# Performance work log

Hardware: AMD Instinct MI355X
Metric: run time of the kernel (lower is better)

The kernel has to match this reference:

```python
import jax, jax.numpy as jnp
import numpy as np

NUM_HEADS = 16
THETA = 10000.0


def setup_inputs() -> dict:
    key = jax.random.key(0)
    k1, k2, k3, k4 = jax.random.split(key, 4)
    B, T, D = 2, 2048, 1024
    x = jax.random.normal(k1, (B, T, D), dtype=jnp.float32)
    token_positions = jnp.sort(
        jax.random.randint(k2, (B, T), 0, 2048), axis=-1
    ).astype(jnp.int32)
    sigma_qkv = float(np.sqrt(2.0 / (D + 3 * D)))
    sigma_out = float(np.sqrt(2.0 / (D + D)))
    W_qkv = jax.random.normal(k3, (3 * D, D), dtype=jnp.float32) * sigma_qkv
    W_out = jax.random.normal(k4, (D, D), dtype=jnp.float32) * sigma_out
    return {"x": x, "token_positions": token_positions, "W_qkv": W_qkv, "W_out": W_out}


def _apply_rope(t, cos, sin):
    # t: [B, H, T, d_k]; cos/sin: [B, T, d_k//2]
    B, H, T, dk = t.shape
    t2 = t.reshape(B, H, T, dk // 2, 2)
    te, to = t2[..., 0], t2[..., 1]
    c = cos[:, None]  # [B, 1, T, dk//2]
    s = sin[:, None]
    ye = te * c - to * s
    yo = to * c + te * s
    return jnp.stack([ye, yo], axis=-1).reshape(B, H, T, dk)


def reference(x, token_positions, W_qkv, W_out):
    B, T, D = x.shape
    H = NUM_HEADS
    dk = D // H

    # fused QKV projection: [B, T, 3D] -> split (three, h, d) on last dim
    qkv = jnp.einsum("btd,od->bto", x, W_qkv).reshape(B, T, 3, H, dk)
    qkv = jnp.transpose(qkv, (2, 0, 3, 1, 4))  # [3, B, H, T, dk]
    q, k, v = qkv[0], qkv[1], qkv[2]

    # RoPE angles from token positions
    n = jnp.arange(dk // 2, dtype=jnp.float32)
    inv_freq = THETA ** (-2.0 * n / dk)  # [dk//2]
    angles = token_positions.astype(jnp.float32)[..., None] * inv_freq  # [B, T, dk//2]
    cos, sin = jnp.cos(angles), jnp.sin(angles)
    q = _apply_rope(q, cos, sin)
    k = _apply_rope(k, cos, sin)

    # causal scaled dot-product attention
    scores = jnp.einsum("bhid,bhjd->bhij", q, k) / jnp.sqrt(jnp.float32(dk))
    causal = jnp.tril(jnp.ones((T, T), dtype=bool))
    scores = jnp.where(causal, scores, -jnp.inf)
    probs = jax.nn.softmax(scores, axis=-1)
    attn = jnp.einsum("bhij,bhjd->bhid", probs, v)  # [B, H, T, dk]

    concat = jnp.transpose(attn, (0, 2, 1, 3)).reshape(B, T, D)
    return jnp.einsum("btd,od->bto", concat, W_out)
```

## Files before the change

### kernel.cpp

```cpp
#include <hip/hip_runtime.h>
#include <hip/hip_bf16.h>
#include <cmath>

#define T_SEQ 2048
#define D_MODEL 1024
#define NHEAD 16
#define DK 64

typedef short bf16x8 __attribute__((ext_vector_type(8)));
typedef float f32x4 __attribute__((ext_vector_type(4)));
typedef float f32x16 __attribute__((ext_vector_type(16)));
typedef unsigned uint2v __attribute__((ext_vector_type(2)));

union U8 { unsigned u[4]; bf16x8 v; };

__device__ __forceinline__ short f2b(float f) {
    unsigned u = __builtin_bit_cast(unsigned, f);
    unsigned r = (u + 0x7FFFu + ((u >> 16) & 1u)) >> 16;
    return (short)r;
}

__device__ __forceinline__ void gll16(const void* g, void* l) {
    __builtin_amdgcn_global_load_lds(
        (__attribute__((address_space(1))) void*)g,
        (__attribute__((address_space(3))) void*)l, 16, 0, 0);
}

__device__ __forceinline__ bf16x8 lds_frag(const short* base, int row, int chunk) {
    return *reinterpret_cast<const bf16x8*>(
        (const char*)base + row * 128 + ((chunk * 16) ^ ((row & 7) << 4)));
}

__device__ __forceinline__ unsigned pkbf16(float a, float b) {
    unsigned r;
    asm("v_cvt_pk_bf16_f32 %0, %1, %2" : "=v"(r) : "v"(a), "v"(b));
    return r;
}
__device__ __forceinline__ void pl32swap(unsigned& a, unsigned& b) {
    uint2v r = __builtin_amdgcn_permlane32_swap(a, b, false, false);
    a = r.x; b = r.y;
}

__global__ __launch_bounds__(256) void cvt_all(const float* __restrict__ x,
                                               const float* __restrict__ wq,
                                               const float* __restrict__ wo,
                                               short* __restrict__ xb,
                                               short* __restrict__ wqb,
                                               short* __restrict__ wob) {
    int i = blockIdx.x * 256 + threadIdx.x;
    const float* src;
    short* dst;
    int srcoff, c;
    if (i < 524288) {
        c = i;
        int tile = c >> 9, cc = c & 511;
        int kblk = cc >> 7, row = cc & 127;
        int rb = tile >> 5, kb = tile & 31;
        srcoff = (rb * 128 + row) * D_MODEL + kb * 32 + kblk * 8;
        src = x; dst = xb;
    } else if (i < 917504) {
        c = i - 524288;
        int tile = c >> 9, cc = c & 511;
        int kblk = cc >> 7, row = cc & 127;
        int rb = tile >> 5, kb = tile & 31;
        srcoff = (rb * 128 + row) * D_MODEL + kb * 32 + kblk * 8;
        src = wq; dst = wqb;
    } else {
        c = i - 917504;
        int tile = c >> 8, cc = c & 255;
        int kblk = cc >> 6, row = cc & 63;
        int nb = tile >> 5, kb = tile & 31;
        srcoff = (nb * 64 + row) * D_MODEL + kb * 32 + kblk * 8;
        src = wo; dst = wob;
    }
    float4 a = *reinterpret_cast<const float4*>(src + srcoff);
    float4 b = *reinterpret_cast<const float4*>(src + srcoff + 4);
    bf16x8 v;
    v[0] = f2b(a.x); v[1] = f2b(a.y); v[2] = f2b(a.z); v[3] = f2b(a.w);
    v[4] = f2b(b.x); v[5] = f2b(b.y); v[6] = f2b(b.z); v[7] = f2b(b.w);
    reinterpret_cast<bf16x8*>(dst)[c] = v;
}

__global__ __launch_bounds__(256) void rope_table(const int* __restrict__ pos,
                                                  float* __restrict__ ct,
                                                  float* __restrict__ st) {
    int i = blockIdx.x * blockDim.x + threadIdx.x;
    int bt = i >> 5, n = i & 31;
    float p = (float)pos[bt];
    float invf = expf((float)n * (-2.0f / (float)DK) * 9.210340371976184f);
    float ang = p * invf;
    float s, c;
    sincosf(ang, &s, &c);
    ct[i] = c; st[i] = s;
}

__global__ __launch_bounds__(256, 3) void gemm_qkv(const short* __restrict__ xb,
                                                   const short* __restrict__ wb,
                                                   const float* __restrict__ ct,
                                                   const float* __restrict__ st,
                                                   short* __restrict__ Qo,
                                                   short* __restrict__ Ko,
                                                   short* __restrict__ Vt) {
    __shared__ short As[2][4096];
    __shared__ short Bs[2][4096];
    const int tid = threadIdx.x;
    const int w = tid >> 6, l = tid & 63, lg = l >> 4, li = l & 15;
    const int wr = w >> 1, wc = w & 1;
    const int bn = blockIdx.x * 128, bm = blockIdx.y * 128;

    const short* pA = xb + (size_t)blockIdx.y * 32 * 4096 + (w * 128 + l) * 8;
    const short* pB = wb + (size_t)blockIdx.x * 32 * 4096 + (w * 128 + l) * 8;

    f32x4 zero = {0.f, 0.f, 0.f, 0.f};
    f32x4 acc[4][4];
#pragma unroll
    for (int m = 0; m < 4; ++m)
#pragma unroll
        for (int n = 0; n < 4; ++n) acc[m][n] = zero;

    gll16(pA,       &As[0][w * 1024]);
    gll16(pA + 512, &As[0][w * 1024 + 512]);
    gll16(pB,       &Bs[0][w * 1024]);
    gll16(pB + 512, &Bs[0][w * 1024 + 512]);
    __syncthreads();

    for (int t = 0; t < 32; ++t) {
        if (t < 31) {
            const int nb = (t + 1) & 1;
            const size_t ko = (size_t)(t + 1) * 4096;
            gll16(pA + ko,       &As[nb][w * 1024]);
            gll16(pA + ko + 512, &As[nb][w * 1024 + 512]);
            gll16(pB + ko,       &Bs[nb][w * 1024]);
            gll16(pB + ko + 512, &Bs[nb][w * 1024 + 512]);
        }
        const int cb = t & 1;
        bf16x8 a[4], b[4];
#pragma unroll
        for (int m = 0; m < 4; ++m)
            a[m] = *reinterpret_cast<const bf16x8*>(&As[cb][lg * 1024 + (wr * 64 + m * 16 + li) * 8]);
#pragma unroll
        for (int n = 0; n < 4; ++n)
            b[n] = *reinterpret_cast<const bf16x8*>(&Bs[cb][lg * 1024 + (wc * 64 + n * 16 + li) * 8]);
#pragma unroll
        for (int m = 0; m < 4; ++m)
#pragma unroll
            for (int n = 0; n < 4; ++n)
                acc[m][n] = __builtin_amdgcn_mfma_f32_16x16x32_bf16(a[m], b[n], acc[m][n], 0, 0, 0);
        __syncthreads();
    }

    const int which = bn >> 10;
    const int h = ((bn >> 6) + wc) & 15;
#pragma unroll
    for (int n = 0; n < 4; ++n) {
        const int d = n * 16 + li;
#pragma unroll
        for (int m = 0; m < 4; ++m)
#pragma unroll
            for (int r = 0; r < 4; ++r) {
                const int mi = bm + wr * 64 + m * 16 + lg * 4 + r;
                const int b_ = mi >> 11, tt = mi & (T_SEQ - 1);
                float v = acc[m][n][r];
                if (which == 2) {
                    Vt[((size_t)((b_ * NHEAD + h) * DK + d)) * T_SEQ + tt] = f2b(v);
                } else {
                    float vp = __shfl_xor(v, 1);
                    int nn = n * 8 + (li >> 1);
                    float c = ct[(size_t)mi * 32 + nn];
                    float s = st[(size_t)mi * 32 + nn];
                    float o = (d & 1) ? (v * c + vp * s) : (v * c - vp * s);
                    if (which == 0) o *= 0.18033688011112042f;
                    short* dst = (which == 0) ? Qo : Ko;
                    dst[((size_t)((b_ * NHEAD + h) * T_SEQ + tt)) * DK + d] = f2b(o);
                }
            }
    }
}

__global__ __launch_bounds__(256, 3) void attn(const short* __restrict__ Q,
                                               const short* __restrict__ K,
                                               const short* __restrict__ Vt,
                                               short* __restrict__ Cc) {
    __shared__ short Kls[2][4096];
    __shared__ short Vls[2][4096];

    const int bid = blockIdx.x;
    const int ii = bid & 255, rr = bid >> 8;
    const int bh = ii & 31;
    const int qt = rr ? (15 - (ii >> 5)) : (ii >> 5);
    const int blkq0 = qt * 128;
    const int ntb = 2 * qt + 2;

    const int tid = threadIdx.x;
    const int w = tid >> 6, l = tid & 63;
    const int l31 = l & 31, hi = l >> 5, hi4 = hi * 4, hi8 = hi * 8;
    const int q0w = blkq0 + w * 32;

    const short* Qh = Q + (size_t)bh * T_SEQ * DK;
    const short* Kh = K + (size_t)bh * T_SEQ * DK;
    const short* Vh = Vt + (size_t)bh * DK * T_SEQ;

    bf16x8 qf[4];
#pragma unroll
    for (int ks = 0; ks < 4; ++ks)
        qf[ks] = *reinterpret_cast<const bf16x8*>(&Qh[(size_t)(q0w + l31) * DK + ks * 16 + hi8]);

    f32x16 o0 = {0.f,0.f,0.f,0.f,0.f,0.f,0.f,0.f,0.f,0.f,0.f,0.f,0.f,0.f,0.f,0.f};
    f32x16 o1 = o0;
    float m = -3.0e38f;
    float lsum = 0.f;

    const int c0 = (2 * w) * 64 + l;
    const int c1 = c0 + 64;
    const int r0 = c0 >> 3, cc0 = (c0 & 7) ^ (r0 & 7);
    const int r1 = c1 >> 3, cc1 = (c1 & 7) ^ (r1 & 7);

#define STAGE(buf, n0_)                                                        \
    do {                                                                       \
        gll16(Kh + (size_t)((n0_) + r0) * DK + cc0 * 8, &Kls[buf][(2 * w) * 512]);      \
        gll16(Kh + (size_t)((n0_) + r1) * DK + cc1 * 8, &Kls[buf][(2 * w + 1) * 512]);  \
        gll16(Vh + (size_t)r0 * T_SEQ + (n0_) + cc0 * 8, &Vls[buf][(2 * w) * 512]);     \
        gll16(Vh + (size_t)r1 * T_SEQ + (n0_) + cc1 * 8, &Vls[buf][(2 * w + 1) * 512]); \
    } while (0)

    STAGE(0, 0);
    __syncthreads();

    for (int t = 0; t < ntb; ++t) {
        const int n0 = t * 64;
        if (t + 1 < ntb) STAGE((t + 1) & 1, (t + 1) * 64);

        if (n0 < q0w + 32) {
            const short* Kc = Kls[t & 1];
            const short* Vc = Vls[t & 1];

            f32x16 s0 = {0.f,0.f,0.f,0.f,0.f,0.f,0.f,0.f,0.f,0.f,0.f,0.f,0.f,0.f,0.f,0.f};
            f32x16 s1 = s0;
            __builtin_amdgcn_s_setprio(1);
#pragma unroll
            for (int ks = 0; ks < 4; ++ks) {
                bf16x8 kf0 = lds_frag(Kc, l31,      ks * 2 + hi);
                bf16x8 kf1 = lds_frag(Kc, 32 + l31, ks * 2 + hi);
                s0 = __builtin_amdgcn_mfma_f32_32x32x16_bf16(kf0, qf[ks], s0, 0, 0, 0);
                s1 = __builtin_amdgcn_mfma_f32_32x32x16_bf16(kf1, qf[ks], s1, 0, 0, 0);
            }
            __builtin_amdgcn_s_setprio(0);

            float p[32];
#pragma unroll
            for (int r = 0; r < 16; ++r) { p[r] = s0[r]; p[16 + r] = s1[r]; }

            if (n0 + 64 > q0w) {
                const int qrel = q0w + l31 - n0;
#pragma unroll
                for (int r = 0; r < 16; ++r) {
                    const int kvm = (r & 3) + 8 * (r >> 2) + hi4;
                    if (kvm > qrel) p[r] = -3.0e38f;
                    if (kvm + 32 > qrel) p[16 + r] = -3.0e38f;
                }
            }

            float t16[16];
#pragma unroll
            for (int r = 0; r < 16; ++r) t16[r] = fmaxf(p[r], p[16 + r]);
#pragma unroll
            for (int d = 8; d >= 1; d >>= 1)
#pragma unroll
                for (int r = 0; r < 8; ++r)
                    if (r < d) t16[r] = fmaxf(t16[r], t16[r + d]);
            float tmax = fmaxf(t16[0], __shfl_xor(t16[0], 32));

            if (__any(tmax > m + 8.0f)) {
                float mnew = fmaxf(m, tmax);
                float alpha = __builtin_amdgcn_exp2f(m - mnew);
                m = mnew;
#pragma unroll
                for (int r = 0; r < 16; ++r) {
                    float ar = __shfl(alpha, (r & 3) + 8 * (r >> 2) + hi4);
                    o0[r] *= ar; o1[r] *= ar;
                }
                lsum *= alpha;
            }

#pragma unroll
            for (int r = 0; r < 32; ++r) p[r] = __builtin_amdgcn_exp2f(p[r] - m);
            float a16[16];
#pragma unroll
            for (int r = 0; r < 16; ++r) a16[r] = p[r] + p[16 + r];
#pragma unroll
            for (int d = 8; d >= 1; d >>= 1)
#pragma unroll
                for (int r = 0; r < 8; ++r)
                    if (r < d) a16[r] += a16[r + d];
            lsum += a16[0] + __shfl_xor(a16[0], 32);

            __builtin_amdgcn_s_setprio(1);
#pragma unroll
            for (int kb = 0; kb < 2; ++kb) {
                unsigned pk0 = pkbf16(p[kb * 16 + 0],  p[kb * 16 + 1]);
                unsigned pk1 = pkbf16(p[kb * 16 + 2],  p[kb * 16 + 3]);
                unsigned pk2 = pkbf16(p[kb * 16 + 4],  p[kb * 16 + 5]);
                unsigned pk3 = pkbf16(p[kb * 16 + 6],  p[kb * 16 + 7]);
                unsigned pk4 = pkbf16(p[kb * 16 + 8],  p[kb * 16 + 9]);
                unsigned pk5 = pkbf16(p[kb * 16 + 10], p[kb * 16 + 11]);
                unsigned pk6 = pkbf16(p[kb * 16 + 12], p[kb * 16 + 13]);
                unsigned pk7 = pkbf16(p[kb * 16 + 14], p[kb * 16 + 15]);
                pl32swap(pk0, pk2); pl32swap(pk1, pk3);
                pl32swap(pk4, pk6); pl32swap(pk5, pk7);
                U8 f0, f1;
                f0.u[0] = pk0; f0.u[1] = pk1; f0.u[2] = pk2; f0.u[3] = pk3;
                f1.u[0] = pk4; f1.u[1] = pk5; f1.u[2] = pk6; f1.u[3] = pk7;
                bf16x8 v00 = lds_frag(Vc, l31,      kb * 4 + hi);
                bf16x8 v01 = lds_frag(Vc, l31,      kb * 4 + 2 + hi);
                bf16x8 v10 = lds_frag(Vc, 32 + l31, kb * 4 + hi);
                bf16x8 v11 = lds_frag(Vc, 32 + l31, kb * 4 + 2 + hi);
                o0 = __builtin_amdgcn_mfma_f32_32x32x16_bf16(f0.v, v00, o0, 0, 0, 0);
                o0 = __builtin_amdgcn_mfma_f32_32x32x16_bf16(f1.v, v01, o0, 0, 0, 0);
                o1 = __builtin_amdgcn_mfma_f32_32x32x16_bf16(f0.v, v10, o1, 0, 0, 0);
                o1 = __builtin_amdgcn_mfma_f32_32x32x16_bf16(f1.v, v11, o1, 0, 0, 0);
            }
            __builtin_amdgcn_s_setprio(0);
        }
        __syncthreads();
    }

    const int b = bh >> 4, h = bh & 15;
    const float linv = 1.0f / lsum;
#pragma unroll
    for (int r = 0; r < 16; ++r) {
        const int qoff = (r & 3) + 8 * (r >> 2) + hi4;
        float inv = __shfl(linv, qoff);
        const int mg = b * T_SEQ + q0w + qoff;
        const int mb = mg >> 7, row = mg & 127;
        const int kblk = (l31 >> 3) & 3, el = l & 7;
        Cc[((size_t)(mb * 32 + h * 2 + 0)) * 4096 + kblk * 1024 + row * 8 + el] = f2b(o0[r] * inv);
        Cc[((size_t)(mb * 32 + h * 2 + 1)) * 4096 + kblk * 1024 + row * 8 + el] = f2b(o1[r] * inv);
    }
}

__global__ __launch_bounds__(256, 3) void gemm_out(const short* __restrict__ ab,
                                                   const short* __restrict__ wb,
                                                   float* __restrict__ out) {
    __shared__ short As[2][4096];
    __shared__ short Bs[2][2048];
    const int tid = threadIdx.x;
    const int w = tid >> 6, l = tid & 63, lg = l >> 4, li = l & 15;
    const int wr = w >> 1, wc = w & 1;
    const int bn = blockIdx.x * 64, bm = blockIdx.y * 128;

    const short* pA = ab + (size_t)blockIdx.y * 32 * 4096 + (w * 128 + l) * 8;
    const short* pB = wb + (size_t)blockIdx.x * 32 * 2048 + (w * 64 + l) * 8;

    f32x4 zero = {0.f, 0.f, 0.f, 0.f};
    f32x4 acc[4][2];
#pragma unroll
    for (int m = 0; m < 4; ++m)
#pragma unroll
        for (int n = 0; n < 2; ++n) acc[m][n] = zero;

    gll16(pA,       &As[0][w * 1024]);
    gll16(pA + 512, &As[0][w * 1024 + 512]);
    gll16(pB,       &Bs[0][w * 512]);
    __syncthreads();

    for (int t = 0; t < 32; ++t) {
        if (t < 31) {
            const int nb = (t + 1) & 1;
            gll16(pA + (size_t)(t + 1) * 4096,       &As[nb][w * 1024]);
            gll16(pA + (size_t)(t + 1) * 4096 + 512, &As[nb][w * 1024 + 512]);
            gll16(pB + (size_t)(t + 1) * 2048,       &Bs[nb][w * 512]);
        }
        const int cb = t & 1;
        bf16x8 a[4], b[2];
#pragma unroll
        for (int m = 0; m < 4; ++m)
            a[m] = *reinterpret_cast<const bf16x8*>(&As[cb][lg * 1024 + (wr * 64 + m * 16 + li) * 8]);
#pragma unroll
        for (int n = 0; n < 2; ++n)
            b[n] = *reinterpret_cast<const bf16x8*>(&Bs[cb][lg * 512 + (wc * 32 + n * 16 + li) * 8]);
#pragma unroll
        for (int m = 0; m < 4; ++m)
#pragma unroll
            for (int n = 0; n < 2; ++n)
                acc[m][n] = __builtin_amdgcn_mfma_f32_16x16x32_bf16(a[m], b[n], acc[m][n], 0, 0, 0);
        __syncthreads();
    }

#pragma unroll
    for (int m = 0; m < 4; ++m)
#pragma unroll
        for (int n = 0; n < 2; ++n)
#pragma unroll
            for (int r = 0; r < 4; ++r) {
                const int mi = bm + wr * 64 + m * 16 + lg * 4 + r;
                out[(size_t)mi * D_MODEL + bn + wc * 32 + n * 16 + li] = acc[m][n][r];
            }
}

extern "C" void kernel_launch(void* const* d_in, const int* in_sizes, int n_in,
                              void* d_out, int out_size, void* d_ws, size_t ws_size,
                              hipStream_t stream) {
    const float* x    = (const float*)d_in[0];
    const int*   pos  = (const int*)d_in[1];
    const float* wqkv = (const float*)d_in[2];
    const float* wout = (const float*)d_in[3];
    float* out = (float*)d_out;

    char* ws = (char*)d_ws;
    size_t off = 0;
    short* xb  = (short*)(ws + off); off += (size_t)4096 * 1024 * 2;
    short* wqb = (short*)(ws + off); off += (size_t)3072 * 1024 * 2;
    short* wob = (short*)(ws + off); off += (size_t)1024 * 1024 * 2;
    short* Q   = (short*)(ws + off); off += (size_t)32 * 2048 * 64 * 2;
    short* Kb  = (short*)(ws + off); off += (size_t)32 * 2048 * 64 * 2;
    short* Vt  = (short*)(ws + off); off += (size_t)32 * 64 * 2048 * 2;
    off += 4096;
    short* Cc  = (short*)(ws + off); off += (size_t)4096 * 1024 * 2;
    float* ct  = (float*)(ws + off); off += (size_t)4096 * 32 * 4;
    float* st  = (float*)(ws + off); off += (size_t)4096 * 32 * 4;

    cvt_all<<<4096, 256, 0, stream>>>(x, wqkv, wout, xb, wqb, wob);
    rope_table<<<512, 256, 0, stream>>>(pos, ct, st);
    gemm_qkv<<<dim3(24, 32), 256, 0, stream>>>(xb, wqb, ct, st, Q, Kb, Vt);
    attn<<<512, 256, 0, stream>>>(Q, Kb, Vt, Cc);
    gemm_out<<<dim3(16, 32), 256, 0, stream>>>(Cc, wob, out);
}
```

Baseline: 132.5 us.

## Triple-buffer GEMM and attention loads, fuse rope table, coalesce V transpose

```diff
diff --git a/kernel.cpp b/kernel.cpp
--- a/kernel.cpp
+++ b/kernel.cpp
@@ -14,6 +14,10 @@
 
 union U8 { unsigned u[4]; bf16x8 v; };
 
+#define VMCNT(n) asm volatile("s_waitcnt vmcnt(" #n ")" ::: "memory")
+#define BAR() __builtin_amdgcn_s_barrier()
+#define SFENCE() __builtin_amdgcn_sched_barrier(0)
+
 __device__ __forceinline__ short f2b(float f) {
     unsigned u = __builtin_bit_cast(unsigned, f);
     unsigned r = (u + 0x7FFFu + ((u >> 16) & 1u)) >> 16;
@@ -44,10 +48,23 @@
 __global__ __launch_bounds__(256) void cvt_all(const float* __restrict__ x,
                                                const float* __restrict__ wq,
                                                const float* __restrict__ wo,
+                                               const int* __restrict__ pos,
                                                short* __restrict__ xb,
                                                short* __restrict__ wqb,
-                                               short* __restrict__ wob) {
+                                               short* __restrict__ wob,
+                                               float* __restrict__ ct,
+                                               float* __restrict__ st) {
     int i = blockIdx.x * 256 + threadIdx.x;
+    if (i >= 1048576) {
+        int j = i - 1048576;
+        int bt = j >> 5, n = j & 31;
+        float p = (float)pos[bt];
+        float invf = expf((float)n * (-2.0f / (float)DK) * 9.210340371976184f);
+        float s, c;
+        sincosf(p * invf, &s, &c);
+        ct[j] = c; st[j] = s;
+        return;
+    }
     const float* src;
     short* dst;
     int srcoff, c;
@@ -81,19 +98,6 @@
     reinterpret_cast<bf16x8*>(dst)[c] = v;
 }
 
-__global__ __launch_bounds__(256) void rope_table(const int* __restrict__ pos,
-                                                  float* __restrict__ ct,
-                                                  float* __restrict__ st) {
-    int i = blockIdx.x * blockDim.x + threadIdx.x;
-    int bt = i >> 5, n = i & 31;
-    float p = (float)pos[bt];
-    float invf = expf((float)n * (-2.0f / (float)DK) * 9.210340371976184f);
-    float ang = p * invf;
-    float s, c;
-    sincosf(ang, &s, &c);
-    ct[i] = c; st[i] = s;
-}
-
 __global__ __launch_bounds__(256, 3) void gemm_qkv(const short* __restrict__ xb,
                                                    const short* __restrict__ wb,
                                                    const float* __restrict__ ct,
@@ -101,8 +105,7 @@
                                                    short* __restrict__ Qo,
                                                    short* __restrict__ Ko,
                                                    short* __restrict__ Vt) {
-    __shared__ short As[2][4096];
-    __shared__ short Bs[2][4096];
+    __shared__ short SM[3][8192];
     const int tid = threadIdx.x;
     const int w = tid >> 6, l = tid & 63, lg = l >> 4, li = l & 15;
     const int wr = w >> 1, wc = w & 1;
@@ -118,52 +121,81 @@
 #pragma unroll
         for (int n = 0; n < 4; ++n) acc[m][n] = zero;
 
-    gll16(pA,       &As[0][w * 1024]);
-    gll16(pA + 512, &As[0][w * 1024 + 512]);
-    gll16(pB,       &Bs[0][w * 1024]);
-    gll16(pB + 512, &Bs[0][w * 1024 + 512]);
-    __syncthreads();
+#define GSTAGE(buf, t_)                                               \
+    do {                                                              \
+        const size_t ko = (size_t)(t_) * 4096;                        \
+        gll16(pA + ko,       &SM[buf][w * 1024]);                     \
+        gll16(pA + ko + 512, &SM[buf][w * 1024 + 512]);               \
+        gll16(pB + ko,       &SM[buf][4096 + w * 1024]);              \
+        gll16(pB + ko + 512, &SM[buf][4096 + w * 1024 + 512]);        \
+    } while (0)
+
+    GSTAGE(0, 0);
+    GSTAGE(1, 1);
 
     for (int t = 0; t < 32; ++t) {
-        if (t < 31) {
-            const int nb = (t + 1) & 1;
-            const size_t ko = (size_t)(t + 1) * 4096;
-            gll16(pA + ko,       &As[nb][w * 1024]);
-            gll16(pA + ko + 512, &As[nb][w * 1024 + 512]);
-            gll16(pB + ko,       &Bs[nb][w * 1024]);
-            gll16(pB + ko + 512, &Bs[nb][w * 1024 + 512]);
-        }
-        const int cb = t & 1;
+        if (t < 31) { VMCNT(4); } else { VMCNT(0); }
+        BAR();
+        SFENCE();
+        if (t + 2 < 32) GSTAGE((t + 2) % 3, t + 2);
+        const short* Ac = &SM[t % 3][0];
+        const short* Bc = &SM[t % 3][4096];
         bf16x8 a[4], b[4];
 #pragma unroll
         for (int m = 0; m < 4; ++m)
-            a[m] = *reinterpret_cast<const bf16x8*>(&As[cb][lg * 1024 + (wr * 64 + m * 16 + li) * 8]);
+            a[m] = *reinterpret_cast<const bf16x8*>(&Ac[lg * 1024 + (wr * 64 + m * 16 + li) * 8]);
 #pragma unroll
         for (int n = 0; n < 4; ++n)
-            b[n] = *reinterpret_cast<const bf16x8*>(&Bs[cb][lg * 1024 + (wc * 64 + n * 16 + li) * 8]);
+            b[n] = *reinterpret_cast<const bf16x8*>(&Bc[lg * 1024 + (wc * 64 + n * 16 + li) * 8]);
+        __builtin_amdgcn_s_setprio(1);
 #pragma unroll
         for (int m = 0; m < 4; ++m)
 #pragma unroll
             for (int n = 0; n < 4; ++n)
                 acc[m][n] = __builtin_amdgcn_mfma_f32_16x16x32_bf16(a[m], b[n], acc[m][n], 0, 0, 0);
-        __syncthreads();
-    }
+        __builtin_amdgcn_s_setprio(0);
+    }
+#undef GSTAGE
 
     const int which = bn >> 10;
     const int h = ((bn >> 6) + wc) & 15;
-#pragma unroll
-    for (int n = 0; n < 4; ++n) {
-        const int d = n * 16 + li;
-#pragma unroll
-        for (int m = 0; m < 4; ++m)
-#pragma unroll
-            for (int r = 0; r < 4; ++r) {
-                const int mi = bm + wr * 64 + m * 16 + lg * 4 + r;
-                const int b_ = mi >> 11, tt = mi & (T_SEQ - 1);
-                float v = acc[m][n][r];
-                if (which == 2) {
-                    Vt[((size_t)((b_ * NHEAD + h) * DK + d)) * T_SEQ + tt] = f2b(v);
-                } else {
+    if (which == 2) {
+        __syncthreads();
+        short* scr = &SM[0][0] + w * 4096;
+#pragma unroll
+        for (int n = 0; n < 4; ++n)
+#pragma unroll
+            for (int m = 0; m < 4; ++m)
+#pragma unroll
+                for (int rp = 0; rp < 2; ++rp) {
+                    int d = n * 16 + li;
+                    int t64 = m * 16 + lg * 4 + rp * 2;
+                    unsigned pk = pkbf16(acc[m][n][rp * 2], acc[m][n][rp * 2 + 1]);
+                    *reinterpret_cast<unsigned*>(
+                        (char*)scr + ((d * 128 + t64 * 2) ^ ((d & 7) << 4))) = pk;
+                }
+        const int mi0 = bm + wr * 64;
+        const int b0 = mi0 >> 11, t0 = mi0 & (T_SEQ - 1);
+        short* vbase = Vt + (size_t)(b0 * NHEAD + h) * DK * T_SEQ + t0;
+#pragma unroll
+        for (int db = 0; db < 8; ++db) {
+            int d = db * 8 + (l >> 3);
+            int ch = l & 7;
+            bf16x8 v = *reinterpret_cast<const bf16x8*>(
+                (char*)scr + ((d * 128 + ch * 16) ^ ((d & 7) << 4)));
+            *reinterpret_cast<bf16x8*>(vbase + (size_t)d * T_SEQ + ch * 8) = v;
+        }
+    } else {
+#pragma unroll
+        for (int n = 0; n < 4; ++n) {
+            const int d = n * 16 + li;
+#pragma unroll
+            for (int m = 0; m < 4; ++m)
+#pragma unroll
+                for (int r = 0; r < 4; ++r) {
+                    const int mi = bm + wr * 64 + m * 16 + lg * 4 + r;
+                    const int b_ = mi >> 11, tt = mi & (T_SEQ - 1);
+                    float v = acc[m][n][r];
                     float vp = __shfl_xor(v, 1);
                     int nn = n * 8 + (li >> 1);
                     float c = ct[(size_t)mi * 32 + nn];
@@ -173,16 +205,16 @@
                     short* dst = (which == 0) ? Qo : Ko;
                     dst[((size_t)((b_ * NHEAD + h) * T_SEQ + tt)) * DK + d] = f2b(o);
                 }
-            }
-    }
-}
-
-__global__ __launch_bounds__(256, 3) void attn(const short* __restrict__ Q,
+        }
+    }
+}
+
+__global__ __launch_bounds__(256, 2) void attn(const short* __restrict__ Q,
                                                const short* __restrict__ K,
                                                const short* __restrict__ Vt,
                                                short* __restrict__ Cc) {
-    __shared__ short Kls[2][4096];
-    __shared__ short Vls[2][4096];
+    __shared__ short Kls[3][4096];
+    __shared__ short Vls[3][4096];
 
     const int bid = blockIdx.x;
     const int ii = bid & 255, rr = bid >> 8;
@@ -210,29 +242,32 @@
     float m = -3.0e38f;
     float lsum = 0.f;
 
-    const int c0 = (2 * w) * 64 + l;
+    const int c0 = w * 128 + l;
     const int c1 = c0 + 64;
     const int r0 = c0 >> 3, cc0 = (c0 & 7) ^ (r0 & 7);
     const int r1 = c1 >> 3, cc1 = (c1 & 7) ^ (r1 & 7);
 
-#define STAGE(buf, n0_)                                                        \
-    do {                                                                       \
+#define ASTAGE(buf, n0_)                                                                \
+    do {                                                                                \
         gll16(Kh + (size_t)((n0_) + r0) * DK + cc0 * 8, &Kls[buf][(2 * w) * 512]);      \
         gll16(Kh + (size_t)((n0_) + r1) * DK + cc1 * 8, &Kls[buf][(2 * w + 1) * 512]);  \
         gll16(Vh + (size_t)r0 * T_SEQ + (n0_) + cc0 * 8, &Vls[buf][(2 * w) * 512]);     \
         gll16(Vh + (size_t)r1 * T_SEQ + (n0_) + cc1 * 8, &Vls[buf][(2 * w + 1) * 512]); \
     } while (0)
 
-    STAGE(0, 0);
-    __syncthreads();
+    ASTAGE(0, 0);
+    ASTAGE(1, 64);
 
     for (int t = 0; t < ntb; ++t) {
+        if (t + 1 < ntb) { VMCNT(4); } else { VMCNT(0); }
+        BAR();
+        SFENCE();
+        if (t + 2 < ntb) ASTAGE((t + 2) % 3, (t + 2) * 64);
         const int n0 = t * 64;
-        if (t + 1 < ntb) STAGE((t + 1) & 1, (t + 1) * 64);
 
         if (n0 < q0w + 32) {
-            const short* Kc = Kls[t & 1];
-            const short* Vc = Vls[t & 1];
+            const short* Kc = Kls[t % 3];
+            const short* Vc = Vls[t % 3];
 
             f32x16 s0 = {0.f,0.f,0.f,0.f,0.f,0.f,0.f,0.f,0.f,0.f,0.f,0.f,0.f,0.f,0.f,0.f};
             f32x16 s1 = s0;
@@ -321,8 +356,8 @@
             }
             __builtin_amdgcn_s_setprio(0);
         }
-        __syncthreads();
-    }
+    }
+#undef ASTAGE
 
     const int b = bh >> 4, h = bh & 15;
     const float linv = 1.0f / lsum;
@@ -341,8 +376,7 @@
 __global__ __launch_bounds__(256, 3) void gemm_out(const short* __restrict__ ab,
                                                    const short* __restrict__ wb,
                                                    float* __restrict__ out) {
-    __shared__ short As[2][4096];
-    __shared__ short Bs[2][2048];
+    __shared__ short SM[3][6144];
     const int tid = threadIdx.x;
     const int w = tid >> 6, l = tid & 63, lg = l >> 4, li = l & 15;
     const int wr = w >> 1, wc = w & 1;
@@ -358,33 +392,39 @@
 #pragma unroll
         for (int n = 0; n < 2; ++n) acc[m][n] = zero;
 
-    gll16(pA,       &As[0][w * 1024]);
-    gll16(pA + 512, &As[0][w * 1024 + 512]);
-    gll16(pB,       &Bs[0][w * 512]);
-    __syncthreads();
+#define OSTAGE(buf, t_)                                                  \
+    do {                                                                 \
+        gll16(pA + (size_t)(t_) * 4096,       &SM[buf][w * 1024]);       \
+        gll16(pA + (size_t)(t_) * 4096 + 512, &SM[buf][w * 1024 + 512]); \
+        gll16(pB + (size_t)(t_) * 2048,       &SM[buf][4096 + w * 512]); \
+    } while (0)
+
+    OSTAGE(0, 0);
+    OSTAGE(1, 1);
 
     for (int t = 0; t < 32; ++t) {
-        if (t < 31) {
-            const int nb = (t + 1) & 1;
-            gll16(pA + (size_t)(t + 1) * 4096,       &As[nb][w * 1024]);
-            gll16(pA + (size_t)(t + 1) * 4096 + 512, &As[nb][w * 1024 + 512]);
-            gll16(pB + (size_t)(t + 1) * 2048,       &Bs[nb][w * 512]);
-        }
-        const int cb = t & 1;
+        if (t < 31) { VMCNT(3); } else { VMCNT(0); }
+        BAR();
+        SFENCE();
+        if (t + 2 < 32) OSTAGE((t + 2) % 3, t + 2);
+        const short* Ac = &SM[t % 3][0];
+        const short* Bc = &SM[t % 3][4096];
         bf16x8 a[4], b[2];
 #pragma unroll
         for (int m = 0; m < 4; ++m)
-            a[m] = *reinterpret_cast<const bf16x8*>(&As[cb][lg * 1024 + (wr * 64 + m * 16 + li) * 8]);
+            a[m] = *reinterpret_cast<const bf16x8*>(&Ac[lg * 1024 + (wr * 64 + m * 16 + li) * 8]);
 #pragma unroll
         for (int n = 0; n < 2; ++n)
-            b[n] = *reinterpret_cast<const bf16x8*>(&Bs[cb][lg * 512 + (wc * 32 + n * 16 + li) * 8]);
+            b[n] = *reinterpret_cast<const bf16x8*>(&Bc[lg * 512 + (wc * 32 + n * 16 + li) * 8]);
+        __builtin_amdgcn_s_setprio(1);
 #pragma unroll
         for (int m = 0; m < 4; ++m)
 #pragma unroll
             for (int n = 0; n < 2; ++n)
                 acc[m][n] = __builtin_amdgcn_mfma_f32_16x16x32_bf16(a[m], b[n], acc[m][n], 0, 0, 0);
-        __syncthreads();
-    }
+        __builtin_amdgcn_s_setprio(0);
+    }
+#undef OSTAGE
 
 #pragma unroll
     for (int m = 0; m < 4; ++m)
@@ -419,8 +459,7 @@
     float* ct  = (float*)(ws + off); off += (size_t)4096 * 32 * 4;
     float* st  = (float*)(ws + off); off += (size_t)4096 * 32 * 4;
 
-    cvt_all<<<4096, 256, 0, stream>>>(x, wqkv, wout, xb, wqb, wob);
-    rope_table<<<512, 256, 0, stream>>>(pos, ct, st);
+    cvt_all<<<4608, 256, 0, stream>>>(x, wqkv, wout, pos, xb, wqb, wob, ct, st);
     gemm_qkv<<<dim3(24, 32), 256, 0, stream>>>(xb, wqb, ct, st, Q, Kb, Vt);
     attn<<<512, 256, 0, stream>>>(Q, Kb, Vt, Cc);
     gemm_out<<<dim3(16, 32), 256, 0, stream>>>(Cc, wob, out);
```

Measured after the change: 114.3 us. 1.16x faster.
